# Optimization experiments

Hardware: AMD Instinct MI355X
Metric: run time of the kernel (lower is better)

The kernel has to match this reference:

```python
import jax, jax.numpy as jnp
import numpy as np

E = 5          # num_experts
TEMP = 1.0     # gate temperature


def setup_inputs() -> dict:
    key = jax.random.key(0)
    ks = jax.random.split(key, 12)
    B, C, H, W = 8, 256, 80, 80
    half, quarter = C // 2, C // 4  # 128, 64
    s = lambda fan_in: 1.0 / np.sqrt(fan_in)
    return {
        "x":    jax.random.normal(ks[0], (B, C, H, W), dtype=jnp.float32),
        # gate Linear(C -> E)
        "Wg":   jax.random.uniform(ks[1], (E, C), jnp.float32, -s(C), s(C)),
        "bg":   jax.random.uniform(ks[2], (E,), jnp.float32, -s(C), s(C)),
        # per-expert conv1x1 weights, stacked on expert axis
        "Wrgb": jax.random.uniform(ks[3], (E, half, half), jnp.float32, -s(half), s(half)),
        "brgb": jax.random.uniform(ks[4], (E, half), jnp.float32, -s(half), s(half)),
        "Wtir": jax.random.uniform(ks[5], (E, half, half), jnp.float32, -s(half), s(half)),
        "btir": jax.random.uniform(ks[6], (E, half), jnp.float32, -s(half), s(half)),
        # transform: conv1x1 half->quarter, ReLU, conv1x1 quarter->1
        "Wt1":  jax.random.uniform(ks[7], (E, quarter, half), jnp.float32, -s(half), s(half)),
        "bt1":  jax.random.uniform(ks[8], (E, quarter), jnp.float32, -s(half), s(half)),
        "Wt2":  jax.random.uniform(ks[9], (E, 1, quarter), jnp.float32, -s(quarter), s(quarter)),
        "bt2":  jax.random.uniform(ks[10], (E, 1), jnp.float32, -s(quarter), s(quarter)),
    }


def _gate(x, Wg, bg):
    # AdaptiveAvgPool2d(1) + Flatten + Linear; eval path (no training noise)
    pooled = x.mean(axis=(2, 3))                       # [B, C]
    logits = pooled @ Wg.T + bg                        # [B, E]
    # top-1 mask + masked softmax (argmax == topk(k=1), first index on ties)
    top1 = jnp.argmax(logits, axis=1)                  # [B]
    mask = jax.nn.one_hot(top1, E, dtype=bool)         # [B, E]
    masked = jnp.where(mask, logits, -jnp.inf)
    return jax.nn.softmax(masked / TEMP, axis=1)       # [B, E]


def _experts(x, Wrgb, brgb, Wtir, btir, Wt1, bt1, Wt2, bt2):
    half = x.shape[1] // 2
    xr, xt = x[:, :half], x[:, half:]                  # [B, half, H, W]
    # residual conv1x1 for all experts at once -> [B, E, half, H, W]
    Dr = xr[:, None] + jnp.einsum('bchw,eoc->beohw', xr, Wrgb) + brgb[None, :, :, None, None]
    Dt = xt[:, None] + jnp.einsum('bchw,eoc->beohw', xt, Wtir) + btir[None, :, :, None, None]

    def transform(D):
        h = jax.nn.relu(jnp.einsum('beohw,emo->bemhw', D, Wt1) + bt1[None, :, :, None, None])
        a = jnp.einsum('bemhw,ekm->bekhw', h, Wt2) + bt2[None, :, :, None, None]
        return jax.nn.sigmoid(a)                       # [B, E, 1, H, W]

    return transform(Dr) * Dr + transform(Dt) * Dt     # [B, E, half, H, W]


def reference(x, Wg, bg, Wrgb, brgb, Wtir, btir, Wt1, bt1, Wt2, bt2):
    weights = _gate(x, Wg, bg)                         # [B, E]
    Dfuse = _experts(x, Wrgb, brgb, Wtir, btir, Wt1, bt1, Wt2, bt2)
    # weighted sum over experts -> [B, half, H, W]
    return jnp.einsum('beohw,be->bohw', Dfuse, weights)
```

## Files before the change

### kernel.cpp

```cpp
#include <hip/hip_runtime.h>

#define HW    6400
#define CIN   256
#define HALF  128
#define QUART 64
#define NB    8
#define NE    5

typedef __attribute__((ext_vector_type(8))) short short8;
typedef __attribute__((ext_vector_type(4))) float f32x4;

__device__ __forceinline__ unsigned short f2bf(float f) {
    unsigned u = __builtin_bit_cast(unsigned, f);
    u = (u + 0x7FFFu + ((u >> 16) & 1u)) >> 16;
    return (unsigned short)u;
}
__device__ __forceinline__ float bf2f(unsigned short h) {
    unsigned u = ((unsigned)h) << 16;
    return __builtin_bit_cast(float, u);
}

__global__ void prep_kernel(const float* __restrict__ Wrgb, const float* __restrict__ Wtir,
                            const float* __restrict__ Wt1, unsigned short* __restrict__ bw) {
    for (int i = blockIdx.x * 256 + threadIdx.x; i < 204800; i += gridDim.x * 256) {
        float v;
        if (i < 81920)       v = Wrgb[i];
        else if (i < 163840) v = Wtir[i - 81920];
        else                 v = Wt1[i - 163840];
        bw[i] = f2bf(v);
    }
}

__global__ void pool_kernel(const float* __restrict__ x, float* __restrict__ pooled) {
    int bc = blockIdx.x;
    const float4* p = reinterpret_cast<const float4*>(x + (size_t)bc * HW);
    float s = 0.f;
    for (int i = threadIdx.x; i < HW / 4; i += 256) {
        float4 v = p[i];
        s += (v.x + v.y) + (v.z + v.w);
    }
    for (int off = 32; off > 0; off >>= 1) s += __shfl_down(s, off, 64);
    __shared__ float wsum[4];
    int wid = threadIdx.x >> 6, lane = threadIdx.x & 63;
    if (lane == 0) wsum[wid] = s;
    __syncthreads();
    if (threadIdx.x == 0)
        pooled[bc] = (wsum[0] + wsum[1] + wsum[2] + wsum[3]) * (1.0f / HW);
}

__global__ void gate_kernel(const float* __restrict__ pooled, const float* __restrict__ Wg,
                            const float* __restrict__ bg, int* __restrict__ eidx) {
    int b = blockIdx.x;
    int lane = threadIdx.x;
    float pv[4];
#pragma unroll
    for (int j = 0; j < 4; ++j) pv[j] = pooled[b * CIN + lane * 4 + j];
    float best = -1e30f; int bi = 0;
    for (int e = 0; e < NE; ++e) {
        float part = 0.f;
#pragma unroll
        for (int j = 0; j < 4; ++j) part += pv[j] * Wg[e * CIN + lane * 4 + j];
        for (int off = 32; off > 0; off >>= 1) part += __shfl_down(part, off, 64);
        part = __shfl(part, 0, 64);
        float logit = part + bg[e];
        if (logit > best) { best = logit; bi = e; }
    }
    if (lane == 0) eidx[b] = bi;
}

__launch_bounds__(256, 3)
__global__ void expert_kernel(const float* __restrict__ x,
                              const unsigned short* __restrict__ bW,
                              const float* __restrict__ brgb, const float* __restrict__ btir,
                              const float* __restrict__ bt1,
                              const float* __restrict__ Wt2, const float* __restrict__ bt2,
                              const int* __restrict__ eidx, float* __restrict__ out) {
    __shared__ unsigned short lxr[8192];
    __shared__ unsigned short lxt[8192];
    __shared__ float lh[64 * 68];
    __shared__ float psum[256];
    __shared__ float sfin[128];

    const int b    = blockIdx.y;
    const int p0   = blockIdx.x * 64;
    const int e    = __builtin_amdgcn_readfirstlane(eidx[b]);
    const int t    = threadIdx.x;
    const int w    = __builtin_amdgcn_readfirstlane(t >> 6);
    const int lane = t & 63;
    const int lo   = lane & 15, hi = lane >> 4;

    const unsigned short* bWrgb = bW + (size_t)e * 16384;
    const unsigned short* bWtir = bW + 81920 + (size_t)e * 16384;
    const unsigned short* bWt1  = bW + 163840 + (size_t)e * 8192;

    {
        const int px = t & 63, cb = t >> 6;
        const float* xb = x + (size_t)b * CIN * HW + p0 + px;
        const int li = (px & 15) * 8;
        const int fb = (cb * 4 + (px >> 4)) * 512;
#pragma unroll
        for (int jg = 0; jg < 4; ++jg) {
            unsigned vr[4], vt[4];
#pragma unroll
            for (int jp = 0; jp < 4; ++jp) {
                int ch = cb * 32 + jg * 8 + jp * 2;
                float r0 = xb[(size_t)ch * HW];
                float r1 = xb[(size_t)(ch + 1) * HW];
                float t0 = xb[(size_t)(ch + HALF) * HW];
                float t1 = xb[(size_t)(ch + HALF + 1) * HW];
                vr[jp] = (unsigned)f2bf(r0) | ((unsigned)f2bf(r1) << 16);
                vt[jp] = (unsigned)f2bf(t0) | ((unsigned)f2bf(t1) << 16);
            }
            int si = fb + jg * 128 + li;
            *reinterpret_cast<uint4*>(&lxr[si]) = make_uint4(vr[0], vr[1], vr[2], vr[3]);
            *reinterpret_cast<uint4*>(&lxt[si]) = make_uint4(vt[0], vt[1], vt[2], vt[3]);
        }
    }
    __syncthreads();

    f32x4 cr[2][4], ct[2][4];
    {
        f32x4 z = {0.f, 0.f, 0.f, 0.f};
#pragma unroll
        for (int i = 0; i < 2; ++i)
#pragma unroll
            for (int j = 0; j < 4; ++j) { cr[i][j] = z; ct[i][j] = z; }
    }
#pragma unroll
    for (int kt = 0; kt < 4; ++kt) {
        short8 bR[4], bT[4];
#pragma unroll
        for (int pt = 0; pt < 4; ++pt) {
            bR[pt] = *reinterpret_cast<const short8*>(&lxr[(kt * 4 + pt) * 512 + lane * 8]);
            bT[pt] = *reinterpret_cast<const short8*>(&lxt[(kt * 4 + pt) * 512 + lane * 8]);
        }
#pragma unroll
        for (int rt = 0; rt < 2; ++rt) {
            int row = w * 32 + rt * 16 + lo;
            short8 aR = *reinterpret_cast<const short8*>(&bWrgb[row * 128 + kt * 32 + hi * 8]);
            short8 aT = *reinterpret_cast<const short8*>(&bWtir[row * 128 + kt * 32 + hi * 8]);
#pragma unroll
            for (int pt = 0; pt < 4; ++pt) {
                cr[rt][pt] = __builtin_amdgcn_mfma_f32_16x16x32_bf16(aR, bR[pt], cr[rt][pt], 0, 0, 0);
                ct[rt][pt] = __builtin_amdgcn_mfma_f32_16x16x32_bf16(aT, bT[pt], ct[rt][pt], 0, 0, 0);
            }
        }
    }

    uint2 dbr[2][4], dbt[2][4];
#pragma unroll
    for (int rt = 0; rt < 2; ++rt) {
        int r0c = w * 32 + rt * 16 + hi * 4;
        f32x4 biasR = *reinterpret_cast<const f32x4*>(&brgb[e * HALF + r0c]);
        f32x4 biasT = *reinterpret_cast<const f32x4*>(&btir[e * HALF + r0c]);
        int kt2 = r0c >> 5;
        int lp8 = (((r0c >> 3) & 3) * 16 + lo) * 8 + (r0c & 7);
#pragma unroll
        for (int pt = 0; pt < 4; ++pt) {
            int si = (kt2 * 4 + pt) * 512 + lp8;
            ushort4 xr4 = *reinterpret_cast<const ushort4*>(&lxr[si]);
            ushort4 xt4 = *reinterpret_cast<const ushort4*>(&lxt[si]);
            float xrv[4] = {bf2f(xr4.x), bf2f(xr4.y), bf2f(xr4.z), bf2f(xr4.w)};
            float xtv[4] = {bf2f(xt4.x), bf2f(xt4.y), bf2f(xt4.z), bf2f(xt4.w)};
#pragma unroll
            for (int rg = 0; rg < 4; ++rg) {
                cr[rt][pt][rg] += biasR[rg] + xrv[rg];
                ct[rt][pt][rg] += biasT[rg] + xtv[rg];
            }
            dbr[rt][pt] = make_uint2(
                (unsigned)f2bf(cr[rt][pt][0]) | ((unsigned)f2bf(cr[rt][pt][1]) << 16),
                (unsigned)f2bf(cr[rt][pt][2]) | ((unsigned)f2bf(cr[rt][pt][3]) << 16));
            dbt[rt][pt] = make_uint2(
                (unsigned)f2bf(ct[rt][pt][0]) | ((unsigned)f2bf(ct[rt][pt][1]) << 16),
                (unsigned)f2bf(ct[rt][pt][2]) | ((unsigned)f2bf(ct[rt][pt][3]) << 16));
        }
    }
    __syncthreads();
#pragma unroll
    for (int rt = 0; rt < 2; ++rt) {
        int r0c = w * 32 + rt * 16 + hi * 4;
        int kt2 = r0c >> 5;
        int lp8 = (((r0c >> 3) & 3) * 16 + lo) * 8 + (r0c & 7);
#pragma unroll
        for (int pt = 0; pt < 4; ++pt) {
            int si = (kt2 * 4 + pt) * 512 + lp8;
            *reinterpret_cast<uint2*>(&lxr[si]) = dbr[rt][pt];
            *reinterpret_cast<uint2*>(&lxt[si]) = dbt[rt][pt];
        }
    }
    __syncthreads();

#pragma unroll
    for (int ph = 0; ph < 2; ++ph) {
        const unsigned short* lD = ph == 0 ? lxr : lxt;
        f32x4 chv[4];
        {
            f32x4 z = {0.f, 0.f, 0.f, 0.f};
#pragma unroll
            for (int j = 0; j < 4; ++j) chv[j] = z;
        }
#pragma unroll
        for (int kt = 0; kt < 4; ++kt) {
            int row = w * 16 + lo;
            short8 aH = *reinterpret_cast<const short8*>(&bWt1[row * 128 + kt * 32 + hi * 8]);
#pragma unroll
            for (int pt = 0; pt < 4; ++pt) {
                short8 bD = *reinterpret_cast<const short8*>(&lD[(kt * 4 + pt) * 512 + lane * 8]);
                chv[pt] = __builtin_amdgcn_mfma_f32_16x16x32_bf16(aH, bD, chv[pt], 0, 0, 0);
            }
        }
        int m0 = w * 16 + hi * 4;
        f32x4 b1 = *reinterpret_cast<const f32x4*>(&bt1[e * QUART + m0]);
#pragma unroll
        for (int pt = 0; pt < 4; ++pt) {
            f32x4 hv;
#pragma unroll
            for (int rg = 0; rg < 4; ++rg) hv[rg] = fmaxf(chv[pt][rg] + b1[rg], 0.f);
            int pxw = pt * 16 + lo;
            *reinterpret_cast<f32x4*>(&lh[pxw * 68 + m0]) = hv;
        }
        __syncthreads();
        {
            int pxa = t & 63, m0a = (t >> 6) * 16;
            const float* w2 = Wt2 + e * QUART + m0a;
            const float* hp = &lh[pxa * 68 + m0a];
            float s16 = 0.f;
#pragma unroll
            for (int j = 0; j < 16; ++j) s16 += w2[j] * hp[j];
            psum[(t >> 6) * 64 + pxa] = s16;
        }
        __syncthreads();
        if (t < 64) {
            float a = psum[t] + psum[64 + t] + psum[128 + t] + psum[192 + t] + bt2[e];
            sfin[ph * 64 + t] = 1.f / (1.f + __expf(-a));
        }
        __syncthreads();
    }

#pragma unroll
    for (int rt = 0; rt < 2; ++rt) {
        int r0c = w * 32 + rt * 16 + hi * 4;
#pragma unroll
        for (int pt = 0; pt < 4; ++pt) {
            int pxb = pt * 16 + lo;
            float sr = sfin[pxb], st = sfin[64 + pxb];
            float* op = out + ((size_t)b * HALF + r0c) * HW + p0 + pxb;
#pragma unroll
            for (int rg = 0; rg < 4; ++rg)
                op[(size_t)rg * HW] = sr * cr[rt][pt][rg] + st * ct[rt][pt][rg];
        }
    }
}

extern "C" void kernel_launch(void* const* d_in, const int* in_sizes, int n_in,
                              void* d_out, int out_size, void* d_ws, size_t ws_size,
                              hipStream_t stream) {
    const float* x    = (const float*)d_in[0];
    const float* Wg   = (const float*)d_in[1];
    const float* bg   = (const float*)d_in[2];
    const float* Wrgb = (const float*)d_in[3];
    const float* brgb = (const float*)d_in[4];
    const float* Wtir = (const float*)d_in[5];
    const float* btir = (const float*)d_in[6];
    const float* Wt1  = (const float*)d_in[7];
    const float* bt1  = (const float*)d_in[8];
    const float* Wt2  = (const float*)d_in[9];
    const float* bt2  = (const float*)d_in[10];
    float* out = (float*)d_out;

    float*          pooled = (float*)d_ws;
    int*            eidx   = (int*)((char*)d_ws + 8192);
    unsigned short* bw     = (unsigned short*)((char*)d_ws + 8448);

    prep_kernel<<<200, 256, 0, stream>>>(Wrgb, Wtir, Wt1, bw);
    pool_kernel<<<NB * CIN, 256, 0, stream>>>(x, pooled);
    gate_kernel<<<NB, 64, 0, stream>>>(pooled, Wg, bg, eidx);
    dim3 grid(100, NB);
    expert_kernel<<<grid, 256, 0, stream>>>(x, bw, brgb, btir, bt1, Wt2, bt2, eidx, out);
}
```

Baseline: 140.0 us.

## Fuse pool/prep and gate into neighbors, fold residual into weights, register-level transform

Merges the weight-conversion and pooling kernels into one launch and moves the gating argmax into the expert kernel, which cuts the launch count from four to two. The residual add is folded into the conv weights by adding an identity (+1 on the diagonal), so x no longer has to be re-read from LDS. The second transform stage now reduces in registers with cross-lane shuffles instead of an LDS round-trip, processes the rgb and tir branches together, and removes several barriers. The occupancy hint is raised from 3 to 4. Rounding the identity-augmented weights to bf16 loses precision on the residual path, and every block now recomputes the gate.

```diff
diff --git a/kernel.cpp b/kernel.cpp
--- a/kernel.cpp
+++ b/kernel.cpp
@@ -15,83 +15,70 @@
     u = (u + 0x7FFFu + ((u >> 16) & 1u)) >> 16;
     return (unsigned short)u;
 }
-__device__ __forceinline__ float bf2f(unsigned short h) {
-    unsigned u = ((unsigned)h) << 16;
-    return __builtin_bit_cast(float, u);
-}
-
-__global__ void prep_kernel(const float* __restrict__ Wrgb, const float* __restrict__ Wtir,
-                            const float* __restrict__ Wt1, unsigned short* __restrict__ bw) {
-    for (int i = blockIdx.x * 256 + threadIdx.x; i < 204800; i += gridDim.x * 256) {
-        float v;
-        if (i < 81920)       v = Wrgb[i];
-        else if (i < 163840) v = Wtir[i - 81920];
-        else                 v = Wt1[i - 163840];
-        bw[i] = f2bf(v);
-    }
-}
-
-__global__ void pool_kernel(const float* __restrict__ x, float* __restrict__ pooled) {
-    int bc = blockIdx.x;
-    const float4* p = reinterpret_cast<const float4*>(x + (size_t)bc * HW);
-    float s = 0.f;
-    for (int i = threadIdx.x; i < HW / 4; i += 256) {
-        float4 v = p[i];
-        s += (v.x + v.y) + (v.z + v.w);
-    }
-    for (int off = 32; off > 0; off >>= 1) s += __shfl_down(s, off, 64);
-    __shared__ float wsum[4];
-    int wid = threadIdx.x >> 6, lane = threadIdx.x & 63;
-    if (lane == 0) wsum[wid] = s;
-    __syncthreads();
-    if (threadIdx.x == 0)
-        pooled[bc] = (wsum[0] + wsum[1] + wsum[2] + wsum[3]) * (1.0f / HW);
-}
-
-__global__ void gate_kernel(const float* __restrict__ pooled, const float* __restrict__ Wg,
-                            const float* __restrict__ bg, int* __restrict__ eidx) {
-    int b = blockIdx.x;
-    int lane = threadIdx.x;
-    float pv[4];
-#pragma unroll
-    for (int j = 0; j < 4; ++j) pv[j] = pooled[b * CIN + lane * 4 + j];
-    float best = -1e30f; int bi = 0;
-    for (int e = 0; e < NE; ++e) {
-        float part = 0.f;
-#pragma unroll
-        for (int j = 0; j < 4; ++j) part += pv[j] * Wg[e * CIN + lane * 4 + j];
-        for (int off = 32; off > 0; off >>= 1) part += __shfl_down(part, off, 64);
-        part = __shfl(part, 0, 64);
-        float logit = part + bg[e];
-        if (logit > best) { best = logit; bi = e; }
-    }
-    if (lane == 0) eidx[b] = bi;
-}
-
-__launch_bounds__(256, 3)
+
+__global__ void pool_prep_kernel(const float* __restrict__ x,
+                                 const float* __restrict__ Wrgb, const float* __restrict__ Wtir,
+                                 const float* __restrict__ Wt1,
+                                 float* __restrict__ pooled, unsigned short* __restrict__ bw) {
+    int blk = blockIdx.x;
+    if (blk < NB * CIN) {
+        const float4* p = reinterpret_cast<const float4*>(x + (size_t)blk * HW);
+        float s = 0.f;
+        for (int i = threadIdx.x; i < HW / 4; i += 256) {
+            float4 v = p[i];
+            s += (v.x + v.y) + (v.z + v.w);
+        }
+        for (int off = 32; off > 0; off >>= 1) s += __shfl_down(s, off, 64);
+        __shared__ float wsum[4];
+        int wid = threadIdx.x >> 6, lane = threadIdx.x & 63;
+        if (lane == 0) wsum[wid] = s;
+        __syncthreads();
+        if (threadIdx.x == 0)
+            pooled[blk] = (wsum[0] + wsum[1] + wsum[2] + wsum[3]) * (1.0f / HW);
+    } else {
+        int i0 = (blk - NB * CIN) * 1024 + threadIdx.x;
+#pragma unroll
+        for (int j = 0; j < 4; ++j) {
+            int i = i0 + j * 256;
+            float v;
+            if (i < 81920) {
+                v = Wrgb[i];
+                int m = i & 16383;
+                if ((m >> 7) == (m & 127)) v += 1.0f;
+            } else if (i < 163840) {
+                int k = i - 81920;
+                v = Wtir[k];
+                int m = k & 16383;
+                if ((m >> 7) == (m & 127)) v += 1.0f;
+            } else {
+                v = Wt1[i - 163840];
+            }
+            bw[i] = f2bf(v);
+        }
+    }
+}
+
+__launch_bounds__(256, 4)
 __global__ void expert_kernel(const float* __restrict__ x,
                               const unsigned short* __restrict__ bW,
                               const float* __restrict__ brgb, const float* __restrict__ btir,
                               const float* __restrict__ bt1,
                               const float* __restrict__ Wt2, const float* __restrict__ bt2,
-                              const int* __restrict__ eidx, float* __restrict__ out) {
+                              const float* __restrict__ pooled,
+                              const float* __restrict__ Wg, const float* __restrict__ bg,
+                              float* __restrict__ out) {
     __shared__ unsigned short lxr[8192];
     __shared__ unsigned short lxt[8192];
-    __shared__ float lh[64 * 68];
-    __shared__ float psum[256];
+    __shared__ float psum[512];
     __shared__ float sfin[128];
+    __shared__ int   se;
 
     const int b    = blockIdx.y;
     const int p0   = blockIdx.x * 64;
-    const int e    = __builtin_amdgcn_readfirstlane(eidx[b]);
     const int t    = threadIdx.x;
     const int w    = __builtin_amdgcn_readfirstlane(t >> 6);
     const int lane = t & 63;
     const int lo   = lane & 15, hi = lane >> 4;
-
-    const unsigned short* bWrgb = bW + (size_t)e * 16384;
-    const unsigned short* bWtir = bW + 81920 + (size_t)e * 16384;
-    const unsigned short* bWt1  = bW + 163840 + (size_t)e * 8192;
 
     {
         const int px = t & 63, cb = t >> 6;
@@ -116,7 +103,29 @@
             *reinterpret_cast<uint4*>(&lxt[si]) = make_uint4(vt[0], vt[1], vt[2], vt[3]);
         }
     }
-    __syncthreads();
+
+    if (t < 64) {
+        float pv[4];
+#pragma unroll
+        for (int j = 0; j < 4; ++j) pv[j] = pooled[b * CIN + t * 4 + j];
+        float best = -1e30f; int bi = 0;
+        for (int e = 0; e < NE; ++e) {
+            float part = 0.f;
+#pragma unroll
+            for (int j = 0; j < 4; ++j) part += pv[j] * Wg[e * CIN + t * 4 + j];
+            for (int off = 32; off > 0; off >>= 1) part += __shfl_down(part, off, 64);
+            part = __shfl(part, 0, 64);
+            float logit = part + bg[e];
+            if (logit > best) { best = logit; bi = e; }
+        }
+        if (t == 0) se = bi;
+    }
+    __syncthreads();
+
+    const int e = __builtin_amdgcn_readfirstlane(se);
+    const unsigned short* bWrgb = bW + (size_t)e * 16384;
+    const unsigned short* bWtir = bW + 81920 + (size_t)e * 16384;
+    const unsigned short* bWt1  = bW + 163840 + (size_t)e * 8192;
 
     f32x4 cr[2][4], ct[2][4];
     {
@@ -153,19 +162,12 @@
         int r0c = w * 32 + rt * 16 + hi * 4;
         f32x4 biasR = *reinterpret_cast<const f32x4*>(&brgb[e * HALF + r0c]);
         f32x4 biasT = *reinterpret_cast<const f32x4*>(&btir[e * HALF + r0c]);
-        int kt2 = r0c >> 5;
-        int lp8 = (((r0c >> 3) & 3) * 16 + lo) * 8 + (r0c & 7);
-#pragma unroll
-        for (int pt = 0; pt < 4; ++pt) {
-            int si = (kt2 * 4 + pt) * 512 + lp8;
-            ushort4 xr4 = *reinterpret_cast<const ushort4*>(&lxr[si]);
-            ushort4 xt4 = *reinterpret_cast<const ushort4*>(&lxt[si]);
-            float xrv[4] = {bf2f(xr4.x), bf2f(xr4.y), bf2f(xr4.z), bf2f(xr4.w)};
-            float xtv[4] = {bf2f(xt4.x), bf2f(xt4.y), bf2f(xt4.z), bf2f(xt4.w)};
+#pragma unroll
+        for (int pt = 0; pt < 4; ++pt) {
 #pragma unroll
             for (int rg = 0; rg < 4; ++rg) {
-                cr[rt][pt][rg] += biasR[rg] + xrv[rg];
-                ct[rt][pt][rg] += biasT[rg] + xtv[rg];
+                cr[rt][pt][rg] += biasR[rg];
+                ct[rt][pt][rg] += biasT[rg];
             }
             dbr[rt][pt] = make_uint2(
                 (unsigned)f2bf(cr[rt][pt][0]) | ((unsigned)f2bf(cr[rt][pt][1]) << 16),
@@ -190,52 +192,53 @@
     }
     __syncthreads();
 
-#pragma unroll
-    for (int ph = 0; ph < 2; ++ph) {
-        const unsigned short* lD = ph == 0 ? lxr : lxt;
-        f32x4 chv[4];
-        {
-            f32x4 z = {0.f, 0.f, 0.f, 0.f};
-#pragma unroll
-            for (int j = 0; j < 4; ++j) chv[j] = z;
-        }
-#pragma unroll
-        for (int kt = 0; kt < 4; ++kt) {
-            int row = w * 16 + lo;
-            short8 aH = *reinterpret_cast<const short8*>(&bWt1[row * 128 + kt * 32 + hi * 8]);
-#pragma unroll
-            for (int pt = 0; pt < 4; ++pt) {
-                short8 bD = *reinterpret_cast<const short8*>(&lD[(kt * 4 + pt) * 512 + lane * 8]);
-                chv[pt] = __builtin_amdgcn_mfma_f32_16x16x32_bf16(aH, bD, chv[pt], 0, 0, 0);
-            }
-        }
+    f32x4 chr[4], cht[4];
+    {
+        f32x4 z = {0.f, 0.f, 0.f, 0.f};
+#pragma unroll
+        for (int j = 0; j < 4; ++j) { chr[j] = z; cht[j] = z; }
+    }
+#pragma unroll
+    for (int kt = 0; kt < 4; ++kt) {
+        int row = w * 16 + lo;
+        short8 aH = *reinterpret_cast<const short8*>(&bWt1[row * 128 + kt * 32 + hi * 8]);
+#pragma unroll
+        for (int pt = 0; pt < 4; ++pt) {
+            short8 bDr = *reinterpret_cast<const short8*>(&lxr[(kt * 4 + pt) * 512 + lane * 8]);
+            short8 bDt = *reinterpret_cast<const short8*>(&lxt[(kt * 4 + pt) * 512 + lane * 8]);
+            chr[pt] = __builtin_amdgcn_mfma_f32_16x16x32_bf16(aH, bDr, chr[pt], 0, 0, 0);
+            cht[pt] = __builtin_amdgcn_mfma_f32_16x16x32_bf16(aH, bDt, cht[pt], 0, 0, 0);
+        }
+    }
+
+    {
         int m0 = w * 16 + hi * 4;
-        f32x4 b1 = *reinterpret_cast<const f32x4*>(&bt1[e * QUART + m0]);
-#pragma unroll
-        for (int pt = 0; pt < 4; ++pt) {
-            f32x4 hv;
-#pragma unroll
-            for (int rg = 0; rg < 4; ++rg) hv[rg] = fmaxf(chv[pt][rg] + b1[rg], 0.f);
-            int pxw = pt * 16 + lo;
-            *reinterpret_cast<f32x4*>(&lh[pxw * 68 + m0]) = hv;
-        }
-        __syncthreads();
-        {
-            int pxa = t & 63, m0a = (t >> 6) * 16;
-            const float* w2 = Wt2 + e * QUART + m0a;
-            const float* hp = &lh[pxa * 68 + m0a];
-            float s16 = 0.f;
-#pragma unroll
-            for (int j = 0; j < 16; ++j) s16 += w2[j] * hp[j];
-            psum[(t >> 6) * 64 + pxa] = s16;
-        }
-        __syncthreads();
-        if (t < 64) {
-            float a = psum[t] + psum[64 + t] + psum[128 + t] + psum[192 + t] + bt2[e];
-            sfin[ph * 64 + t] = 1.f / (1.f + __expf(-a));
-        }
-        __syncthreads();
-    }
+        f32x4 b1  = *reinterpret_cast<const f32x4*>(&bt1[e * QUART + m0]);
+        f32x4 w2v = *reinterpret_cast<const f32x4*>(&Wt2[e * QUART + m0]);
+#pragma unroll
+        for (int pt = 0; pt < 4; ++pt) {
+            float pr = 0.f, ptt = 0.f;
+#pragma unroll
+            for (int rg = 0; rg < 4; ++rg) {
+                pr  = fmaf(w2v[rg], fmaxf(chr[pt][rg] + b1[rg], 0.f), pr);
+                ptt = fmaf(w2v[rg], fmaxf(cht[pt][rg] + b1[rg], 0.f), ptt);
+            }
+            pr  += __shfl_xor(pr, 16, 64);  pr  += __shfl_xor(pr, 32, 64);
+            ptt += __shfl_xor(ptt, 16, 64); ptt += __shfl_xor(ptt, 32, 64);
+            if (hi == 0) {
+                psum[w * 64 + pt * 16 + lo]       = pr;
+                psum[256 + w * 64 + pt * 16 + lo] = ptt;
+            }
+        }
+    }
+    __syncthreads();
+    if (t < 128) {
+        int ph = t >> 6, px = t & 63;
+        const float* ps = &psum[ph * 256];
+        float a = ps[px] + ps[64 + px] + ps[128 + px] + ps[192 + px] + bt2[e];
+        sfin[t] = 1.f / (1.f + __expf(-a));
+    }
+    __syncthreads();
 
 #pragma unroll
     for (int rt = 0; rt < 2; ++rt) {
@@ -269,12 +272,10 @@
     float* out = (float*)d_out;
 
     float*          pooled = (float*)d_ws;
-    int*            eidx   = (int*)((char*)d_ws + 8192);
-    unsigned short* bw     = (unsigned short*)((char*)d_ws + 8448);
-
-    prep_kernel<<<200, 256, 0, stream>>>(Wrgb, Wtir, Wt1, bw);
-    pool_kernel<<<NB * CIN, 256, 0, stream>>>(x, pooled);
-    gate_kernel<<<NB, 64, 0, stream>>>(pooled, Wg, bg, eidx);
+    unsigned short* bw     = (unsigned short*)((char*)d_ws + 8192);
+
+    pool_prep_kernel<<<NB * CIN + 200, 256, 0, stream>>>(x, Wrgb, Wtir, Wt1, pooled, bw);
     dim3 grid(100, NB);
-    expert_kernel<<<grid, 256, 0, stream>>>(x, bw, brgb, btir, bt1, Wt2, bt2, eidx, out);
-}
+    expert_kernel<<<grid, 256, 0, stream>>>(x, bw, brgb, btir, bt1, Wt2, bt2,
+                                            pooled, Wg, bg, out);
+}
```

After: 133.3 us (median of 2 runs). -4.8%, faster.
